# Optimization experiments

Measured on AMD Instinct MI355X. Metric: run time of the kernel, lower is better.

The kernel has to match this reference:

```python
import jax, jax.numpy as jnp
import numpy as np
from jax import lax

B, L, D = 1024, 50, 128          # batch, max_seq_len, embed_dim
NV, NH = 8, 16                    # n_v vertical filters, n_h horizontal filters
NU, NI = 100000, 100000           # num_users, num_items


def setup_inputs() -> dict:
    key = jax.random.key(0)
    ks = jax.random.split(key, 9)
    return {
        "user_ids": jax.random.randint(ks[0], (B,), 0, NU),
        "item_seq": jax.random.randint(ks[1], (B, L), 0, NI),
        "user_emb": jax.random.normal(ks[2], (NU, D), jnp.float32) * 0.02,
        "item_emb": jax.random.normal(ks[3], (NI, D), jnp.float32) * 0.02,
        "vfilter": jax.random.normal(ks[4], (L, NV), jnp.float32) * 0.1,
        # hconv_w[i] holds the Conv2d(1, NH, (i+1, D)) weight, zero-padded to height L;
        # only rows [:i+1] are used for filter of height h=i+1.
        "hconv_w": jax.random.normal(ks[5], (L, NH, L, D), jnp.float32) * 0.05,
        "hconv_b": jax.random.normal(ks[6], (L, NH), jnp.float32) * 0.01,
        "fc_w": jax.random.normal(ks[7], (NV * D + NH * L, D), jnp.float32) * 0.02,
        "fc_b": jax.random.normal(ks[8], (D,), jnp.float32) * 0.01,
    }


def reference(user_ids, item_seq, user_emb, item_emb, vfilter, hconv_w, hconv_b, fc_w, fc_b):
    P_u = user_emb[user_ids]                 # [B, D]
    E = item_emb[item_seq]                   # [B, L, D]

    # vertical conv: (E^T @ V)^T flattened as (v major, d minor) -> [B, NV*D]
    o_v = jnp.einsum('bld,lv->bvd', E, vfilter).reshape(E.shape[0], -1)

    # horizontal convs: one per kernel height h = 1..L (structurally distinct kernels)
    x = E[:, None, :, :]                     # NCHW: [B, 1, L, D]
    o_h = []
    for i in range(L):
        h = i + 1
        w = hconv_w[i, :, :h, :][:, None, :, :]   # OIHW: [NH, 1, h, D]
        c = lax.conv_general_dilated(
            x, w, window_strides=(1, 1), padding='VALID',
            dimension_numbers=('NCHW', 'OIHW', 'NCHW'))[..., 0]   # [B, NH, L-h+1]
        c = jax.nn.relu(c + hconv_b[i][None, :, None])
        o_h.append(jnp.max(c, axis=2))            # max-pool over all valid positions
    o_h = jnp.concatenate(o_h, axis=1)            # [B, NH*L]

    o = jnp.concatenate([o_v, o_h], axis=1)       # [B, NV*D + NH*L]
    z = jax.nn.relu(o @ fc_w + fc_b)              # [B, D]
    return jnp.concatenate([z, P_u], axis=1)      # [B, 2*D]
```

## Files before the change

kernel.cpp:

```cpp
#include <hip/hip_runtime.h>
#include <hip/hip_bf16.h>
#include <stdint.h>

#define B_   1024
#define L_   50
#define D_   128
#define NV_  8
#define NH_  16
#define KFC  1824

typedef __bf16 bf16x8 __attribute__((ext_vector_type(8)));
typedef float  f32x4  __attribute__((ext_vector_type(4)));

static __device__ __forceinline__ bf16x8 as_bf16x8(uint4 u) {
  return __builtin_bit_cast(bf16x8, u);
}

static __device__ __forceinline__ unsigned short f2b(float x) {
  unsigned u = __float_as_uint(x);
  return (unsigned short)((u + 0x7FFFu + ((u >> 16) & 1u)) >> 16);
}

#define OV_BYTES  ((size_t)B_ * KFC * 4)
#define E3OFF     (OV_BYTES)
#define E3_BG     52224
#define E3_KS     ((size_t)64 * E3_BG)
#define E3SZ      ((size_t)4 * E3_KS)
#define W2OFF     (E3OFF + E3SZ)
#define W2SZ      ((size_t)1275 * 4096)
#define CTR_OFF   (W2OFF + W2SZ)
#define NEED_FULL (CTR_OFF + 256)

#define GLD16(gsrc, ldst) __builtin_amdgcn_global_load_lds(                    \
    (const __attribute__((address_space(1))) void*)(gsrc),                     \
    (__attribute__((address_space(3))) void*)(ldst), 16, 0, 0)

__global__ void ck_kP(const int* __restrict__ uids, const float* __restrict__ uemb,
                      float* __restrict__ out) {
  int b = blockIdx.x, d = threadIdx.x;
  out[(size_t)b * 256 + 128 + d] = uemb[(size_t)uids[b] * D_ + d];
}

__global__ void ck_kZ(float* __restrict__ out) {
  int i = blockIdx.x * 256 + threadIdx.x;
  int b = i >> 7, d = i & 127;
  out[(size_t)b * 256 + d] = 0.f;
}

__global__ void ck_kAB(const int* __restrict__ item_seq, const float* __restrict__ item_emb,
                       const float* __restrict__ vf, char* __restrict__ ws) {
  int b = blockIdx.x, tid = threadIdx.x;
  __shared__ float E[L_][D_];
  __shared__ float VF[L_][NV_];
  __shared__ int sidx[L_];
  if (tid < L_) sidx[tid] = item_seq[b * L_ + tid];
  for (int c = tid; c < L_ * NV_; c += 256) VF[c / NV_][c % NV_] = vf[c];
  __syncthreads();
  for (int c = tid; c < 1600; c += 256) {
    int l = c >> 5, ch = c & 31;
    *(float4*)&E[l][ch * 4] = *(const float4*)(item_emb + (size_t)sidx[l] * D_ + ch * 4);
  }
  __syncthreads();
  char* eg = ws + E3OFF + (size_t)(b >> 4) * E3_BG + (b & 15) * 64;
  #pragma unroll
  for (int it = 0; it < 4; ++it) {
    int c = it * 256 + tid;
    if (c < 816) {
      int ks = c / 204, rem = c - ks * 204;
      uint4 v = make_uint4(0, 0, 0, 0);
      int row, gq;
      if (rem < 200) {
        row = rem >> 2; gq = rem & 3;
        float4 f0 = *(const float4*)&E[row][ks * 32 + gq * 8];
        float4 f1 = *(const float4*)&E[row][ks * 32 + gq * 8 + 4];
        v.x = f2b(f0.x) | ((unsigned)f2b(f0.y) << 16);
        v.y = f2b(f0.z) | ((unsigned)f2b(f0.w) << 16);
        v.z = f2b(f1.x) | ((unsigned)f2b(f1.y) << 16);
        v.w = f2b(f1.z) | ((unsigned)f2b(f1.w) << 16);
      } else {
        row = 50; gq = rem - 200;
      }
      *(uint4*)(eg + (size_t)ks * E3_KS + row * 1024 + gq * 16) = v;
    }
  }
  int d = tid & 127, half = tid >> 7;
  float acc[4] = {0.f, 0.f, 0.f, 0.f};
  for (int l = 0; l < L_; ++l) {
    float e = E[l][d];
    #pragma unroll
    for (int vv = 0; vv < 4; ++vv) acc[vv] += e * VF[l][half * 4 + vv];
  }
  float* o = (float*)ws + (size_t)b * KFC;
  #pragma unroll
  for (int vv = 0; vv < 4; ++vv) o[(half * 4 + vv) * D_ + d] = acc[vv];
}

__global__ void ck_kW2(const float* __restrict__ hw, char* __restrict__ ws) {
  int p = blockIdx.x, tid = threadIdx.x;
  int ks = tid >> 6, l = tid & 63;
  int n = l & 15, gq = l >> 4;
  int i = (int)((sqrtf(8.0f * (float)p + 1.0f) - 1.0f) * 0.5f);
  while ((i + 1) * (i + 2) / 2 <= p) ++i;
  while (i * (i + 1) / 2 > p) --i;
  int j = p - i * (i + 1) / 2;
  const float* src = hw + ((size_t)(i * 16 + n) * 50 + j) * 128 + ks * 32 + gq * 8;
  float4 f0 = *(const float4*)(src);
  float4 f1 = *(const float4*)(src + 4);
  uint4 v;
  v.x = f2b(f0.x) | ((unsigned)f2b(f0.y) << 16);
  v.y = f2b(f0.z) | ((unsigned)f2b(f0.w) << 16);
  v.z = f2b(f1.x) | ((unsigned)f2b(f1.y) << 16);
  v.w = f2b(f1.z) | ((unsigned)f2b(f1.w) << 16);
  *(uint4*)(ws + W2OFF + (size_t)p * 4096 + tid * 16) = v;
}

#define MFMA_BF16 __builtin_amdgcn_mfma_f32_16x16x32_bf16

__device__ __forceinline__ void proc10(const char* buf, const char* bp0,
    int i, int t0, f32x4 (&acc)[8], int aoff) {
  bf16x8 win[8];
  #pragma unroll
  for (int q = 0; q < 8; ++q) {
    int s = t0 + q; s = s > 50 ? 50 : s;
    win[q] = as_bf16x8(*(const uint4*)(buf + s * 1024 + aoff));
  }
  uint4 breg[8];
  #pragma unroll
  for (int u = 0; u < 8; ++u)
    breg[u] = *(const uint4*)(bp0 + (size_t)(u <= i ? u : 0) * 4096);

  for (int j0 = 0; j0 <= i; j0 += 8) {
    #pragma unroll
    for (int u = 0; u < 8; ++u) {
      int j = j0 + u;
      if (j <= i) {
        bf16x8 bfr = as_bf16x8(breg[u]);
        acc[0] = MFMA_BF16(win[u], bfr, acc[0], 0, 0, 0);
        acc[1] = MFMA_BF16(win[(u + 1) & 7], bfr, acc[1], 0, 0, 0);
        acc[2] = MFMA_BF16(win[(u + 2) & 7], bfr, acc[2], 0, 0, 0);
        acc[3] = MFMA_BF16(win[(u + 3) & 7], bfr, acc[3], 0, 0, 0);
        int sn = t0 + j + 8; sn = sn > 50 ? 50 : sn;
        win[u] = as_bf16x8(*(const uint4*)(buf + sn * 1024 + aoff));
        acc[4] = MFMA_BF16(win[(u + 4) & 7], bfr, acc[4], 0, 0, 0);
        acc[5] = MFMA_BF16(win[(u + 5) & 7], bfr, acc[5], 0, 0, 0);
        acc[6] = MFMA_BF16(win[(u + 6) & 7], bfr, acc[6], 0, 0, 0);
        acc[7] = MFMA_BF16(win[(u + 7) & 7], bfr, acc[7], 0, 0, 0);
        if (j + 8 <= i) breg[u] = *(const uint4*)(bp0 + (size_t)(j + 8) * 4096);
      }
    }
  }
}

__attribute__((amdgpu_waves_per_eu(2, 4)))
__launch_bounds__(512)
__global__ void ck_kC10(const float* __restrict__ hconv_b, char* __restrict__ ws) {
  __shared__ __align__(16) char lds[E3_BG + 16];
  int* bcast = (int*)(lds + E3_BG);
  int tid = threadIdx.x;
  int wv = tid >> 6, lane = tid & 63;
  int r = lane & 15, gq = lane >> 4;
  int g = (int)blockIdx.x;
  int aoff = r * 64 + gq * 16;

  const char* EG = ws + E3OFF + (size_t)g * E3_BG;
  const char* W2 = ws + W2OFF;
  unsigned* ctr = (unsigned*)(ws + CTR_OFF) + g;
  float* o = (float*)ws;

  int ks_in_buf = -1;
  int flip = 0;

  for (;;) {
    if (tid == 0) bcast[0] = (int)atomicAdd(ctr, 8u);
    __syncthreads();
    int base = bcast[0];
    if (base >= 182) break;

    int widx = base + wv;
    int i = -1, nt = 0, t0 = 0;
    int rem = widx;
    for (int ii = 49; ii >= 0; --ii) {
      int nw = (57 - ii) >> 3;
      if (rem < nw) {
        i = ii;
        int ntb = 50 - ii - 8 * (nw - 1);
        nt = rem ? 8 : ntb;
        t0 = rem ? ntb + 8 * (rem - 1) : 0;
        break;
      }
      rem -= nw;
    }

    f32x4 acc[8];
    #pragma unroll
    for (int t = 0; t < 8; ++t) {
      acc[t][0] = 0.f; acc[t][1] = 0.f; acc[t][2] = 0.f; acc[t][3] = 0.f;
    }
    const char* bpb = W2 + (size_t)(i >= 0 ? i * (i + 1) / 2 : 0) * 4096 + lane * 16;

    for (int kk = 0; kk < 4; ++kk) {
      int ks = flip ? (3 - kk) : kk;
      if (ks != ks_in_buf) {
        __syncthreads();
        const char* src = EG + (size_t)ks * E3_KS;
        #pragma unroll
        for (int it = 0; it < 6; ++it)
          GLD16(src + (size_t)(it * 512 + tid) * 16, lds + (it * 512 + wv * 64) * 16);
        if (wv < 3)
          GLD16(src + (size_t)(3072 + tid) * 16, lds + (3072 + wv * 64) * 16);
        __syncthreads();
        ks_in_buf = ks;
      }
      if (i >= 0) proc10(lds, bpb + ks * 1024, i, t0, acc, aoff);
    }
    flip ^= 1;

    if (i >= 0) {
      int b0 = g * 16;
      float bias = hconv_b[i * 16 + r];
      #pragma unroll
      for (int e = 0; e < 4; ++e) {
        float m = 0.f;
        #pragma unroll
        for (int tt = 0; tt < 8; ++tt)
          if (tt < nt) m = fmaxf(m, fmaxf(acc[tt][e] + bias, 0.f));
        atomicMax((unsigned*)&o[(size_t)(b0 + gq * 4 + e) * KFC + 1024 + i * 16 + r],
                  __float_as_uint(m));
      }
    }
    __syncthreads();
  }
}

__launch_bounds__(256)
__global__ void ck_kD(const float* __restrict__ fc_w, const float* __restrict__ fc_b,
                      const char* __restrict__ ws, float* __restrict__ out) {
  __shared__ char ldsD[10240];
  int b0 = blockIdx.x * 64, n0 = blockIdx.y * 16;
  int tid = threadIdx.x, w = tid >> 6, lane = tid & 63, r = lane & 15, gq = lane >> 4;
  const float* o = (const float*)ws;

  f32x4 acc; acc[0] = 0.f; acc[1] = 0.f; acc[2] = 0.f; acc[3] = 0.f;

  int rl = tid >> 2, ch = tid & 3;
  const float* asrc = o + (size_t)(b0 + rl) * KFC + ch * 8;
  int kk = tid >> 3, nn = tid & 7;

  float4 fa[4]; float fb[4];
  fa[0] = *(const float4*)(asrc);
  fa[1] = *(const float4*)(asrc + 4);
  fa[2] = *(const float4*)(asrc + 32);
  fa[3] = *(const float4*)(asrc + 36);
  fb[0] = fc_w[(size_t)kk * D_ + n0 + nn];
  fb[1] = fc_w[(size_t)kk * D_ + n0 + nn + 8];
  fb[2] = fc_w[(size_t)(32 + kk) * D_ + n0 + nn];
  fb[3] = fc_w[(size_t)(32 + kk) * D_ + n0 + nn + 8];

  int arow_off = rl * 64 + ((ch ^ (rl & 3)) << 4);
  int rloc = w * 16 + r;
  int ard = rloc * 64 + ((gq ^ (rloc & 3)) << 4);
  int brd = 8192 + r * 64 + ((gq ^ (r & 3)) << 4);
  int bw0 = 8192 + nn * 64 + (((kk >> 3) ^ (nn & 3)) << 4) + (kk & 7) * 2;
  int bw1 = 8192 + (nn + 8) * 64 + (((kk >> 3) ^ ((nn + 8) & 3)) << 4) + (kk & 7) * 2;

  for (int s = 0; s < 29; ++s) {
    int k1ok = (2 * s + 1) < 57;
    __syncthreads();
    #pragma unroll
    for (int sl = 0; sl < 2; ++sl) {
      uint4 v;
      v.x = f2b(fa[2*sl].x) | ((unsigned)f2b(fa[2*sl].y) << 16);
      v.y = f2b(fa[2*sl].z) | ((unsigned)f2b(fa[2*sl].w) << 16);
      v.z = f2b(fa[2*sl+1].x) | ((unsigned)f2b(fa[2*sl+1].y) << 16);
      v.w = f2b(fa[2*sl+1].z) | ((unsigned)f2b(fa[2*sl+1].w) << 16);
      *(uint4*)(ldsD + sl * 4096 + arow_off) = v;
      *(unsigned short*)(ldsD + sl * 1024 + bw0) = f2b(fb[2*sl]);
      *(unsigned short*)(ldsD + sl * 1024 + bw1) = f2b(fb[2*sl+1]);
    }
    __syncthreads();
    int kn0 = (2 * s + 2) * 32, kn1 = (2 * s + 3) * 32;
    if (kn0 < 1824) {
      fa[0] = *(const float4*)(asrc + kn0);
      fa[1] = *(const float4*)(asrc + kn0 + 4);
      fb[0] = fc_w[(size_t)(kn0 + kk) * D_ + n0 + nn];
      fb[1] = fc_w[(size_t)(kn0 + kk) * D_ + n0 + nn + 8];
    }
    if (kn1 < 1824) {
      fa[2] = *(const float4*)(asrc + kn1);
      fa[3] = *(const float4*)(asrc + kn1 + 4);
      fb[2] = fc_w[(size_t)(kn1 + kk) * D_ + n0 + nn];
      fb[3] = fc_w[(size_t)(kn1 + kk) * D_ + n0 + nn + 8];
    }
    bf16x8 a0  = as_bf16x8(*(const uint4*)(ldsD + ard));
    bf16x8 b0f = as_bf16x8(*(const uint4*)(ldsD + brd));
    acc = __builtin_amdgcn_mfma_f32_16x16x32_bf16(a0, b0f, acc, 0, 0, 0);
    if (k1ok) {
      bf16x8 a1  = as_bf16x8(*(const uint4*)(ldsD + 4096 + ard));
      bf16x8 b1f = as_bf16x8(*(const uint4*)(ldsD + 1024 + brd));
      acc = __builtin_amdgcn_mfma_f32_16x16x32_bf16(a1, b1f, acc, 0, 0, 0);
    }
  }

  float bias = fc_b[n0 + r];
  #pragma unroll
  for (int e = 0; e < 4; ++e) {
    int row = b0 + w * 16 + gq * 4 + e;
    out[(size_t)row * 256 + n0 + r] = fmaxf(acc[e] + bias, 0.f);
  }
}

extern "C" void kernel_launch(void* const* d_in, const int* in_sizes, int n_in,
                              void* d_out, int out_size, void* d_ws, size_t ws_size,
                              hipStream_t stream) {
  const int*   user_ids = (const int*)d_in[0];
  const int*   item_seq = (const int*)d_in[1];
  const float* user_emb = (const float*)d_in[2];
  const float* item_emb = (const float*)d_in[3];
  const float* vfilter  = (const float*)d_in[4];
  const float* hconv_w  = (const float*)d_in[5];
  const float* hconv_b  = (const float*)d_in[6];
  const float* fc_w     = (const float*)d_in[7];
  const float* fc_b     = (const float*)d_in[8];
  float* out = (float*)d_out;
  char*  ws  = (char*)d_ws;

  ck_kP<<<dim3(B_), dim3(128), 0, stream>>>(user_ids, user_emb, out);

  if (ws_size < NEED_FULL) {
    ck_kZ<<<dim3(512), dim3(256), 0, stream>>>(out);
    return;
  }

  hipMemsetAsync(ws, 0, OV_BYTES, stream);
  hipMemsetAsync(ws + CTR_OFF, 0, 256, stream);

  ck_kAB<<<dim3(B_), dim3(256), 0, stream>>>(item_seq, item_emb, vfilter, ws);
  ck_kW2<<<dim3(1275), dim3(256), 0, stream>>>(hconv_w, ws);
  ck_kC10<<<dim3(64, 8), dim3(512), 0, stream>>>(hconv_b, ws);
  ck_kD<<<dim3(16, 8), dim3(256), 0, stream>>>(fc_w, fc_b, ws, out);
}
```

Before: 176.5 us.

## Replace atomic work queue with static cost-sorted schedule in hconv kernel

The horizontal-conv kernel no longer pulls work through a global atomic counter. Each block now builds, in LDS, a schedule that ranks the 182 window tasks by cost (kernel height) and deals them serpentine-style across 64 wave slots over 3 rounds. This removes the counter memset, the per-iteration atomic with its broadcast barrier, and the trailing syncthreads. It also folds the user-embedding copy into the embedding-gather kernel to save a launch, moves the B-fragment prefetch earlier, adds a sched_barrier, and sets launch bounds to 2 blocks per CU. The static balance could be worse than the dynamic queue if costs are not proportional to height.

```diff
diff --git a/kernel.cpp b/kernel.cpp
--- a/kernel.cpp
+++ b/kernel.cpp
@@ -28,8 +28,7 @@
 #define E3SZ      ((size_t)4 * E3_KS)
 #define W2OFF     (E3OFF + E3SZ)
 #define W2SZ      ((size_t)1275 * 4096)
-#define CTR_OFF   (W2OFF + W2SZ)
-#define NEED_FULL (CTR_OFF + 256)
+#define NEED_FULL (W2OFF + W2SZ)
 
 #define GLD16(gsrc, ldst) __builtin_amdgcn_global_load_lds(                    \
     (const __attribute__((address_space(1))) void*)(gsrc),                     \
@@ -47,14 +46,18 @@
   out[(size_t)b * 256 + d] = 0.f;
 }
 
-__global__ void ck_kAB(const int* __restrict__ item_seq, const float* __restrict__ item_emb,
-                       const float* __restrict__ vf, char* __restrict__ ws) {
+__global__ void ck_kABP(const int* __restrict__ user_ids, const int* __restrict__ item_seq,
+                        const float* __restrict__ user_emb, const float* __restrict__ item_emb,
+                        const float* __restrict__ vf, char* __restrict__ ws,
+                        float* __restrict__ out) {
   int b = blockIdx.x, tid = threadIdx.x;
   __shared__ float E[L_][D_];
   __shared__ float VF[L_][NV_];
   __shared__ int sidx[L_];
   if (tid < L_) sidx[tid] = item_seq[b * L_ + tid];
   for (int c = tid; c < L_ * NV_; c += 256) VF[c / NV_][c % NV_] = vf[c];
+  if (tid < 128)
+    out[(size_t)b * 256 + 128 + tid] = user_emb[(size_t)user_ids[b] * D_ + tid];
   __syncthreads();
   for (int c = tid; c < 1600; c += 256) {
     int l = c >> 5, ch = c & 31;
@@ -115,8 +118,12 @@
 }
 
 #define MFMA_BF16 __builtin_amdgcn_mfma_f32_16x16x32_bf16
-
-__device__ __forceinline__ void proc10(const char* buf, const char* bp0,
+#define NWIN 182
+#define WCOST_OFF E3_BG
+#define SCHED_OFF (E3_BG + 736)
+#define LDS_TOT   (E3_BG + 736 + 768)
+
+__device__ __forceinline__ void proc12(const char* buf, const char* bp0,
     int i, int t0, f32x4 (&acc)[8], int aoff) {
   bf16x8 win[8];
   #pragma unroll
@@ -141,55 +148,65 @@
         acc[3] = MFMA_BF16(win[(u + 3) & 7], bfr, acc[3], 0, 0, 0);
         int sn = t0 + j + 8; sn = sn > 50 ? 50 : sn;
         win[u] = as_bf16x8(*(const uint4*)(buf + sn * 1024 + aoff));
+        if (j + 8 <= i) breg[u] = *(const uint4*)(bp0 + (size_t)(j + 8) * 4096);
         acc[4] = MFMA_BF16(win[(u + 4) & 7], bfr, acc[4], 0, 0, 0);
         acc[5] = MFMA_BF16(win[(u + 5) & 7], bfr, acc[5], 0, 0, 0);
         acc[6] = MFMA_BF16(win[(u + 6) & 7], bfr, acc[6], 0, 0, 0);
         acc[7] = MFMA_BF16(win[(u + 7) & 7], bfr, acc[7], 0, 0, 0);
-        if (j + 8 <= i) breg[u] = *(const uint4*)(bp0 + (size_t)(j + 8) * 4096);
+        __builtin_amdgcn_sched_barrier(0x20F);
       }
     }
   }
 }
 
-__attribute__((amdgpu_waves_per_eu(2, 4)))
-__launch_bounds__(512)
-__global__ void ck_kC10(const float* __restrict__ hconv_b, char* __restrict__ ws) {
-  __shared__ __align__(16) char lds[E3_BG + 16];
-  int* bcast = (int*)(lds + E3_BG);
+__launch_bounds__(512, 2)
+__global__ void ck_kC12(const float* __restrict__ hconv_b, char* __restrict__ ws) {
+  __shared__ __align__(16) char lds[LDS_TOT];
+  int* wcost = (int*)(lds + WCOST_OFF);
+  int* sched = (int*)(lds + SCHED_OFF);
   int tid = threadIdx.x;
   int wv = tid >> 6, lane = tid & 63;
   int r = lane & 15, gq = lane >> 4;
   int g = (int)blockIdx.x;
+  int slot = (int)blockIdx.y * 8 + wv;
   int aoff = r * 64 + gq * 16;
 
   const char* EG = ws + E3OFF + (size_t)g * E3_BG;
   const char* W2 = ws + W2OFF;
-  unsigned* ctr = (unsigned*)(ws + CTR_OFF) + g;
   float* o = (float*)ws;
+
+  if (tid < 192) sched[tid] = -1;
+  int myenc = -1;
+  if (tid < NWIN) {
+    int idx = tid, i, nw = 1;
+    for (i = 0; i < 50; ++i) {
+      nw = (57 - i) >> 3;
+      if (idx < nw) break;
+      idx -= nw;
+    }
+    int ntb = 50 - i - 8 * (nw - 1);
+    int nt = idx ? 8 : ntb;
+    int t0 = idx ? ntb + 8 * (idx - 1) : 0;
+    myenc = i | (t0 << 8) | (nt << 16);
+    wcost[tid] = ((i + 1) << 8) + tid;
+  }
+  __syncthreads();
+  if (tid < NWIN) {
+    int c = wcost[tid], rank = 0;
+    for (int u = 0; u < NWIN; ++u) rank += (wcost[u] > c) ? 1 : 0;
+    int rnd = rank >> 6, pos = rank & 63;
+    int sl = (rnd & 1) ? (63 - pos) : pos;
+    sched[sl * 3 + rnd] = myenc;
+  }
+  __syncthreads();
 
   int ks_in_buf = -1;
   int flip = 0;
 
-  for (;;) {
-    if (tid == 0) bcast[0] = (int)atomicAdd(ctr, 8u);
-    __syncthreads();
-    int base = bcast[0];
-    if (base >= 182) break;
-
-    int widx = base + wv;
-    int i = -1, nt = 0, t0 = 0;
-    int rem = widx;
-    for (int ii = 49; ii >= 0; --ii) {
-      int nw = (57 - ii) >> 3;
-      if (rem < nw) {
-        i = ii;
-        int ntb = 50 - ii - 8 * (nw - 1);
-        nt = rem ? 8 : ntb;
-        t0 = rem ? ntb + 8 * (rem - 1) : 0;
-        break;
-      }
-      rem -= nw;
-    }
+  for (int rd = 0; rd < 3; ++rd) {
+    int enc = sched[slot * 3 + rd];
+    int i = -1, t0 = 0, nt = 0;
+    if (enc >= 0) { i = enc & 0xff; t0 = (enc >> 8) & 0xff; nt = (enc >> 16) & 0xff; }
 
     f32x4 acc[8];
     #pragma unroll
@@ -211,7 +228,7 @@
         __syncthreads();
         ks_in_buf = ks;
       }
-      if (i >= 0) proc10(lds, bpb + ks * 1024, i, t0, acc, aoff);
+      if (i >= 0) proc12(lds, bpb + ks * 1024, i, t0, acc, aoff);
     }
     flip ^= 1;
 
@@ -228,7 +245,6 @@
                   __float_as_uint(m));
       }
     }
-    __syncthreads();
   }
 }
 
@@ -324,18 +340,17 @@
   float* out = (float*)d_out;
   char*  ws  = (char*)d_ws;
 
-  ck_kP<<<dim3(B_), dim3(128), 0, stream>>>(user_ids, user_emb, out);
-
   if (ws_size < NEED_FULL) {
+    ck_kP<<<dim3(B_), dim3(128), 0, stream>>>(user_ids, user_emb, out);
     ck_kZ<<<dim3(512), dim3(256), 0, stream>>>(out);
     return;
   }
 
   hipMemsetAsync(ws, 0, OV_BYTES, stream);
-  hipMemsetAsync(ws + CTR_OFF, 0, 256, stream);
-
-  ck_kAB<<<dim3(B_), dim3(256), 0, stream>>>(item_seq, item_emb, vfilter, ws);
+
+  ck_kABP<<<dim3(B_), dim3(256), 0, stream>>>(user_ids, item_seq, user_emb,
+                                              item_emb, vfilter, ws, out);
   ck_kW2<<<dim3(1275), dim3(256), 0, stream>>>(hconv_w, ws);
-  ck_kC10<<<dim3(64, 8), dim3(512), 0, stream>>>(hconv_b, ws);
+  ck_kC12<<<dim3(64, 8), dim3(512), 0, stream>>>(hconv_b, ws);
   ck_kD<<<dim3(16, 8), dim3(256), 0, stream>>>(fc_w, fc_b, ws, out);
 }
```

New measurement: 184.9 us. 4.8% more time.
